# Performance work log

Measured on AMD Instinct MI355X. Metric: run time of the kernel, lower is better.

## Reference

```python
import jax, jax.numpy as jnp
import numpy as np
import math

N, M, D = 16384, 4096, 256
RATIO = 0.5
EDGE_PROB = 0.005  # ~80 nodes per hyperedge on average


def setup_inputs() -> dict:
    key = jax.random.key(0)
    k0, k1, k2, k3 = jax.random.split(key, 4)
    node_features = jax.random.normal(k0, (N, D), dtype=jnp.float32)
    # sparse-ish 0/1 incidence matrix, stored dense as in the original module
    incidence = (jax.random.uniform(k1, (N, M)) < EDGE_PROB).astype(jnp.float32)
    node_mask = jnp.ones((N,), dtype=bool)
    edge_mask = jnp.ones((M,), dtype=bool)
    W = (jax.random.normal(k2, (D, D)) / np.sqrt(D)).astype(jnp.float32)
    b = jnp.zeros((D,), dtype=jnp.float32)
    proj = (jax.random.normal(k3, (D,)) * 0.01).astype(jnp.float32)
    return dict(node_features=node_features, incidence=incidence,
                node_mask=node_mask, edge_mask=edge_mask,
                W=W, b=b, proj=proj)


def reference(node_features, incidence, node_mask, edge_mask, W, b, proj):
    n = node_features.shape[0]
    k = max(1, math.ceil(RATIO * n))  # static

    # --- UniGCNConv: node -> edge mean, edge -> node mean, then linear ---
    deg_e = jnp.clip(jnp.sum(incidence, axis=0), 1.0)          # [m]
    x_edge = (incidence.T @ node_features) / deg_e[:, None]     # [m, d]
    deg_v = jnp.clip(jnp.sum(incidence, axis=1), 1.0)           # [n]
    agg = (incidence @ x_edge) / deg_v[:, None]                 # [n, d]
    embeddings = agg @ W + b                                    # [n, d]

    # --- learned scalar score per node ---
    scores = jax.nn.sigmoid(embeddings @ proj)                  # [n]
    scores = jnp.where(node_mask, scores, -jnp.inf)

    # --- full argsort top-k -> boolean node mask (as in original) ---
    ranked = jnp.argsort(-scores)
    top_k_indices = ranked[:k]
    new_node_mask = jnp.zeros(n, dtype=jnp.bool_).at[top_k_indices].set(True)

    # --- gate features by score ---
    gated_features = node_features * scores[:, None]            # [n, d]

    # --- incidence masked-reduce -> active edges ---
    active_membership = incidence * new_node_mask[:, None].astype(incidence.dtype)
    edge_active_count = jnp.sum(active_membership, axis=0)      # [m]
    new_edge_mask = (edge_active_count > 0) & edge_mask

    return gated_features, new_node_mask, new_edge_mask
```

## Files before the change

kernel.cpp:

```cpp
#include <hip/hip_runtime.h>
#include <stdint.h>
#include <math.h>

#define N_NODES 16384
#define M_EDGES 4096
#define DFEAT   256
#define KSEL    8192
#define ECAP    192
#define VCAP    96


__global__ void build_lists(const float* __restrict__ inc,
                            int* __restrict__ ecnt, int* __restrict__ vcnt,
                            uint16_t* __restrict__ elist, uint16_t* __restrict__ vlist) {
    long long idx = (long long)blockIdx.x * blockDim.x + threadIdx.x;
    const long long total4 = (long long)N_NODES * M_EDGES / 4;
    if (idx >= total4) return;
    long long e = idx * 4;
    int n  = (int)(e >> 12);
    int m0 = (int)(e & 4095);
    const float4 v = ((const float4*)inc)[idx];
    float vals[4] = {v.x, v.y, v.z, v.w};
#pragma unroll
    for (int j = 0; j < 4; ++j) {
        if (vals[j] != 0.0f) {
            int m  = m0 + j;
            int ei = atomicAdd(&ecnt[m], 1);
            if (ei < ECAP) elist[(long long)m * ECAP + ei] = (uint16_t)n;
            int vi = atomicAdd(&vcnt[n], 1);
            if (vi < VCAP) vlist[(long long)n * VCAP + vi] = (uint16_t)m;
        }
    }
}

__global__ void compute_w2(const float* __restrict__ W, const float* __restrict__ b,
                           const float* __restrict__ proj, double* __restrict__ w2,
                           double* __restrict__ bp) {
    int d = threadIdx.x;
    double acc = 0.0;
    for (int j = 0; j < DFEAT; ++j)
        acc += (double)W[d * DFEAT + j] * (double)proj[j];
    w2[d] = acc;
    if (d == 0) {
        double s = 0.0;
        for (int j = 0; j < DFEAT; ++j) s += (double)b[j] * (double)proj[j];
        *bp = s;
    }
}

__global__ void z_kernel(const float* __restrict__ X, const double* __restrict__ w2,
                         double* __restrict__ z) {
    int wave = threadIdx.x >> 6;
    int lane = threadIdx.x & 63;
    int n = blockIdx.x * 4 + wave;
    float4 x = ((const float4*)X)[n * 64 + lane];
    int j = lane * 4;
    double acc = (double)x.x * w2[j] + (double)x.y * w2[j + 1]
               + (double)x.z * w2[j + 2] + (double)x.w * w2[j + 3];
    for (int o = 32; o > 0; o >>= 1) acc += __shfl_down(acc, o, 64);
    if (lane == 0) z[n] = acc;
}

__global__ void y_kernel(const double* __restrict__ z, const int* __restrict__ ecnt,
                         const uint16_t* __restrict__ elist, double* __restrict__ y) {
    int wave = threadIdx.x >> 6;
    int lane = threadIdx.x & 63;
    int m = blockIdx.x * 4 + wave;
    int cntr = ecnt[m];
    int cnt = cntr > ECAP ? ECAP : cntr;
    const uint16_t* lst = elist + (long long)m * ECAP;
    double acc = 0.0;
    for (int i = lane; i < cnt; i += 64) acc += z[lst[i]];
    for (int o = 32; o > 0; o >>= 1) acc += __shfl_down(acc, o, 64);
    if (lane == 0) {
        double deg = cntr > 0 ? (double)cntr : 1.0;
        y[m] = acc / deg;
    }
}

__global__ void logit_kernel(const double* __restrict__ y, const int* __restrict__ vcnt,
                             const uint16_t* __restrict__ vlist, const double* __restrict__ bp,
                             unsigned long long* __restrict__ keys, float* __restrict__ scores) {
    int n = blockIdx.x * blockDim.x + threadIdx.x;
    if (n >= N_NODES) return;
    int cntr = vcnt[n];
    int cnt = cntr > VCAP ? VCAP : cntr;
    const uint16_t* lst = vlist + (long long)n * VCAP;
    double acc = 0.0;
    for (int i = 0; i < cnt; ++i) acc += y[lst[i]];
    double deg = cntr > 0 ? (double)cntr : 1.0;
    double logit = acc / deg + *bp;
    scores[n] = (float)(1.0 / (1.0 + exp(-logit)));
    unsigned long long u = (unsigned long long)__double_as_longlong(logit);
    u = (u >> 63) ? ~u : (u | 0x8000000000000000ull);
    keys[n] = u;
}

__global__ __launch_bounds__(1024) void radix_select(
        const unsigned long long* __restrict__ keys, unsigned long long* __restrict__ Tu) {
    int tid = threadIdx.x;
    int wave = tid >> 6, lane = tid & 63;
    unsigned long long k[16];
#pragma unroll
    for (int i = 0; i < 16; ++i) k[i] = keys[i * 1024 + tid];
    __shared__ unsigned long long wsum[2][16];
    unsigned long long prefix = 0ull;
    int kr = KSEL;
    int par = 0;
    for (int shift = 62; shift >= 0; shift -= 2, par ^= 1) {
        unsigned long long base = prefix >> shift;
        int c3 = 0, c2 = 0, c1 = 0;
#pragma unroll
        for (int i = 0; i < 16; ++i) {
            unsigned long long hi = k[i] >> shift;
            c3 += (hi == base + 3);
            c2 += (hi == base + 2);
            c1 += (hi == base + 1);
        }
        unsigned long long packed = (unsigned long long)c3
                                  | ((unsigned long long)c2 << 21)
                                  | ((unsigned long long)c1 << 42);
        for (int o = 32; o > 0; o >>= 1) packed += __shfl_down(packed, o, 64);
        if (lane == 0) wsum[par][wave] = packed;
        __syncthreads();
        unsigned long long tot = 0;
#pragma unroll
        for (int w = 0; w < 16; ++w) tot += wsum[par][w];
        int n3 = (int)(tot & 0x1FFFFF);
        int n2 = (int)((tot >> 21) & 0x1FFFFF);
        int n1 = (int)((tot >> 42) & 0x1FFFFF);
        if (kr <= n3) prefix |= 3ull << shift;
        else { kr -= n3;
            if (kr <= n2) prefix |= 2ull << shift;
            else { kr -= n2;
                if (kr <= n1) prefix |= 1ull << shift;
                else kr -= n1;
            }
        }
    }
    if (tid == 0) *Tu = prefix;
}

__global__ __launch_bounds__(1024) void build_mask(
        const unsigned long long* __restrict__ keys, const unsigned long long* __restrict__ Tu,
        float* __restrict__ out_mask, int* __restrict__ maski) {
    int tid = threadIdx.x;
    int wave = tid >> 6, lane = tid & 63;
    unsigned long long T = *Tu;
    unsigned long long k[16];
#pragma unroll
    for (int i = 0; i < 16; ++i) k[i] = keys[tid * 16 + i];
    int ceq = 0, cgt = 0;
#pragma unroll
    for (int i = 0; i < 16; ++i) { cgt += (k[i] > T); ceq += (k[i] == T); }
    int eq_incl = ceq;
    for (int o = 1; o < 64; o <<= 1) {
        int v = __shfl_up(eq_incl, o, 64);
        if (lane >= o) eq_incl += v;
    }
    int gt_sum = cgt;
    for (int o = 32; o > 0; o >>= 1) gt_sum += __shfl_down(gt_sum, o, 64);
    __shared__ int weq[16], wgt[16];
    if (lane == 63) weq[wave] = eq_incl;
    if (lane == 0)  wgt[wave] = gt_sum;
    __syncthreads();
    int base_eq = 0, tot_gt = 0;
#pragma unroll
    for (int w = 0; w < 16; ++w) {
        if (w < wave) base_eq += weq[w];
        tot_gt += wgt[w];
    }
    int need = KSEL - tot_gt;
    int r = base_eq + eq_incl - ceq;
#pragma unroll
    for (int i = 0; i < 16; ++i) {
        bool eq = (k[i] == T);
        bool sel = (k[i] > T) || (eq && r < need);
        if (eq) ++r;
        int idx = tid * 16 + i;
        out_mask[idx] = sel ? 1.0f : 0.0f;
        maski[idx] = sel ? 1 : 0;
    }
}

__global__ void gated_out(const float* __restrict__ X, const float* __restrict__ scores,
                          float* __restrict__ out) {
    int idx = blockIdx.x * blockDim.x + threadIdx.x;
    int n = idx >> 6;
    float s = scores[n];
    float4 v = ((const float4*)X)[idx];
    v.x *= s; v.y *= s; v.z *= s; v.w *= s;
    ((float4*)out)[idx] = v;
}

__global__ void edge_mask_out(const int* __restrict__ ecnt, const uint16_t* __restrict__ elist,
                              const int* __restrict__ maski, float* __restrict__ out) {
    int m = blockIdx.x * blockDim.x + threadIdx.x;
    if (m >= M_EDGES) return;
    int cnt = ecnt[m]; if (cnt > ECAP) cnt = ECAP;
    const uint16_t* lst = elist + (long long)m * ECAP;
    int active = 0;
    for (int i = 0; i < cnt; ++i) {
        if (maski[lst[i]]) { active = 1; break; }
    }
    out[m] = active ? 1.0f : 0.0f;
}

extern "C" void kernel_launch(void* const* d_in, const int* in_sizes, int n_in,
                              void* d_out, int out_size, void* d_ws, size_t ws_size,
                              hipStream_t stream) {
    const float* X    = (const float*)d_in[0];
    const float* inc  = (const float*)d_in[1];
    const float* W    = (const float*)d_in[4];
    const float* b    = (const float*)d_in[5];
    const float* proj = (const float*)d_in[6];

    char* ws = (char*)d_ws;
    int*                ecnt   = (int*)(ws + 0);
    int*                vcnt   = (int*)(ws + 16384);
    double*             w2     = (double*)(ws + 81920);
    double*             bp     = (double*)(ws + 83968);
    unsigned long long* Tu     = (unsigned long long*)(ws + 83976);
    unsigned long long* keys   = (unsigned long long*)(ws + 131072);
    float*              scores = (float*)(ws + 262144);
    int*                maski  = (int*)(ws + 327680);
    double*             z      = (double*)(ws + 393216);
    double*             y      = (double*)(ws + 524288);
    uint16_t*           elist  = (uint16_t*)(ws + 4587520);
    uint16_t*           vlist  = (uint16_t*)(ws + 6160384);

    float* out_gated = (float*)d_out;
    float* out_nmask = out_gated + (long long)N_NODES * DFEAT;
    float* out_emask = out_nmask + N_NODES;

    hipMemsetAsync(ws, 0, 81920, stream);

    const long long total4 = (long long)N_NODES * M_EDGES / 4;
    build_lists<<<(int)(total4 / 256), 256, 0, stream>>>(inc, ecnt, vcnt, elist, vlist);
    compute_w2<<<1, 256, 0, stream>>>(W, b, proj, w2, bp);
    z_kernel<<<N_NODES / 4, 256, 0, stream>>>(X, w2, z);
    y_kernel<<<M_EDGES / 4, 256, 0, stream>>>(z, ecnt, elist, y);
    logit_kernel<<<N_NODES / 256, 256, 0, stream>>>(y, vcnt, vlist, bp, keys, scores);
    radix_select<<<1, 1024, 0, stream>>>(keys, Tu);
    build_mask<<<1, 1024, 0, stream>>>(keys, Tu, out_nmask, maski);
    gated_out<<<(N_NODES * DFEAT / 4) / 256, 256, 0, stream>>>(X, scores, out_gated);
    edge_mask_out<<<(M_EDGES + 255) / 256, 256, 0, stream>>>(ecnt, elist, maski, out_emask);
}
```

Measured before the change: 539.4 us.

## Fuse edge aggregation into row-wise incidence scan with atomic z accumulation

Replaces the per-element list builder plus per-edge gather with a single row-per-block kernel. It scans incidence, atomically accumulates node scalars into edge sums, and writes node adjacency lists using a wave prefix scan instead of per-node atomics. The edge list and separate y kernel are removed, and the edge mask is computed by scattering from selected nodes. The trade-off is contended fp64 atomics on edge sums and a summation order that is no longer deterministic.

```diff
diff --git a/kernel.cpp b/kernel.cpp
--- a/kernel.cpp
+++ b/kernel.cpp
@@ -6,32 +6,8 @@
 #define M_EDGES 4096
 #define DFEAT   256
 #define KSEL    8192
-#define ECAP    192
 #define VCAP    96
 
-
-__global__ void build_lists(const float* __restrict__ inc,
-                            int* __restrict__ ecnt, int* __restrict__ vcnt,
-                            uint16_t* __restrict__ elist, uint16_t* __restrict__ vlist) {
-    long long idx = (long long)blockIdx.x * blockDim.x + threadIdx.x;
-    const long long total4 = (long long)N_NODES * M_EDGES / 4;
-    if (idx >= total4) return;
-    long long e = idx * 4;
-    int n  = (int)(e >> 12);
-    int m0 = (int)(e & 4095);
-    const float4 v = ((const float4*)inc)[idx];
-    float vals[4] = {v.x, v.y, v.z, v.w};
-#pragma unroll
-    for (int j = 0; j < 4; ++j) {
-        if (vals[j] != 0.0f) {
-            int m  = m0 + j;
-            int ei = atomicAdd(&ecnt[m], 1);
-            if (ei < ECAP) elist[(long long)m * ECAP + ei] = (uint16_t)n;
-            int vi = atomicAdd(&vcnt[n], 1);
-            if (vi < VCAP) vlist[(long long)n * VCAP + vi] = (uint16_t)m;
-        }
-    }
-}
 
 __global__ void compute_w2(const float* __restrict__ W, const float* __restrict__ b,
                            const float* __restrict__ proj, double* __restrict__ w2,
@@ -61,24 +37,63 @@
     if (lane == 0) z[n] = acc;
 }
 
-__global__ void y_kernel(const double* __restrict__ z, const int* __restrict__ ecnt,
-                         const uint16_t* __restrict__ elist, double* __restrict__ y) {
-    int wave = threadIdx.x >> 6;
-    int lane = threadIdx.x & 63;
-    int m = blockIdx.x * 4 + wave;
-    int cntr = ecnt[m];
-    int cnt = cntr > ECAP ? ECAP : cntr;
-    const uint16_t* lst = elist + (long long)m * ECAP;
-    double acc = 0.0;
-    for (int i = lane; i < cnt; i += 64) acc += z[lst[i]];
-    for (int o = 32; o > 0; o >>= 1) acc += __shfl_down(acc, o, 64);
-    if (lane == 0) {
-        double deg = cntr > 0 ? (double)cntr : 1.0;
-        y[m] = acc / deg;
-    }
-}
-
-__global__ void logit_kernel(const double* __restrict__ y, const int* __restrict__ vcnt,
+__global__ void build(const float* __restrict__ inc, const double* __restrict__ z,
+                      int* __restrict__ ecnt, int* __restrict__ vcnt,
+                      double* __restrict__ ysum, uint16_t* __restrict__ vlist) {
+    int n = blockIdx.x;
+    int t = threadIdx.x;
+    int lane = t & 63, wv = t >> 6;
+    const float4* row4 = (const float4*)inc + (long long)n * 1024;
+    unsigned bits = 0;
+#pragma unroll
+    for (int c = 0; c < 4; ++c) {
+        float4 v = row4[c * 256 + t];
+        unsigned b = (v.x != 0.0f ? 1u : 0u) | (v.y != 0.0f ? 2u : 0u)
+                   | (v.z != 0.0f ? 4u : 0u) | (v.w != 0.0f ? 8u : 0u);
+        bits |= b << (c * 4);
+    }
+    double zn = z[n];
+    unsigned bb = bits;
+    while (bb) {
+        int k = __ffs(bb) - 1;
+        bb &= bb - 1;
+        int m = ((k >> 2) << 10) + t * 4 + (k & 3);
+        atomicAdd(&ysum[m], zn);
+        atomicAdd(&ecnt[m], 1);
+    }
+    int h = __popc(bits);
+    int incl = h;
+    for (int o = 1; o < 64; o <<= 1) {
+        int v = __shfl_up(incl, o, 64);
+        if (lane >= o) incl += v;
+    }
+    __shared__ int wtot[4];
+    if (lane == 63) wtot[wv] = incl;
+    __syncthreads();
+    int base = incl - h;
+#pragma unroll
+    for (int w = 0; w < 4; ++w) if (w < wv) base += wtot[w];
+    if (t == 0) vcnt[n] = wtot[0] + wtot[1] + wtot[2] + wtot[3];
+    uint16_t* vrow = vlist + (long long)n * VCAP;
+    int s = base;
+    while (bits) {
+        int k = __ffs(bits) - 1;
+        bits &= bits - 1;
+        int m = ((k >> 2) << 10) + t * 4 + (k & 3);
+        if (s < VCAP) vrow[s] = (uint16_t)m;
+        ++s;
+    }
+}
+
+__global__ void ymean_kernel(const double* __restrict__ ysum, const int* __restrict__ ecnt,
+                             double* __restrict__ ymean) {
+    int m = blockIdx.x * blockDim.x + threadIdx.x;
+    if (m >= M_EDGES) return;
+    int c = ecnt[m];
+    ymean[m] = ysum[m] / (c > 0 ? (double)c : 1.0);
+}
+
+__global__ void logit_kernel(const double* __restrict__ ymean, const int* __restrict__ vcnt,
                              const uint16_t* __restrict__ vlist, const double* __restrict__ bp,
                              unsigned long long* __restrict__ keys, float* __restrict__ scores) {
     int n = blockIdx.x * blockDim.x + threadIdx.x;
@@ -87,7 +102,7 @@
     int cnt = cntr > VCAP ? VCAP : cntr;
     const uint16_t* lst = vlist + (long long)n * VCAP;
     double acc = 0.0;
-    for (int i = 0; i < cnt; ++i) acc += y[lst[i]];
+    for (int i = 0; i < cnt; ++i) acc += ymean[lst[i]];
     double deg = cntr > 0 ? (double)cntr : 1.0;
     double logit = acc / deg + *bp;
     scores[n] = (float)(1.0 / (1.0 + exp(-logit)));
@@ -193,17 +208,14 @@
     ((float4*)out)[idx] = v;
 }
 
-__global__ void edge_mask_out(const int* __restrict__ ecnt, const uint16_t* __restrict__ elist,
-                              const int* __restrict__ maski, float* __restrict__ out) {
-    int m = blockIdx.x * blockDim.x + threadIdx.x;
-    if (m >= M_EDGES) return;
-    int cnt = ecnt[m]; if (cnt > ECAP) cnt = ECAP;
-    const uint16_t* lst = elist + (long long)m * ECAP;
-    int active = 0;
-    for (int i = 0; i < cnt; ++i) {
-        if (maski[lst[i]]) { active = 1; break; }
-    }
-    out[m] = active ? 1.0f : 0.0f;
+__global__ void emask_scatter(const int* __restrict__ maski, const int* __restrict__ vcnt,
+                              const uint16_t* __restrict__ vlist, float* __restrict__ out) {
+    int n = blockIdx.x * blockDim.x + threadIdx.x;
+    if (n >= N_NODES || !maski[n]) return;
+    int cntr = vcnt[n];
+    int cnt = cntr > VCAP ? VCAP : cntr;
+    const uint16_t* lst = vlist + (long long)n * VCAP;
+    for (int i = 0; i < cnt; ++i) out[lst[i]] = 1.0f;
 }
 
 extern "C" void kernel_launch(void* const* d_in, const int* in_sizes, int n_in,
@@ -218,31 +230,31 @@
     char* ws = (char*)d_ws;
     int*                ecnt   = (int*)(ws + 0);
     int*                vcnt   = (int*)(ws + 16384);
-    double*             w2     = (double*)(ws + 81920);
-    double*             bp     = (double*)(ws + 83968);
-    unsigned long long* Tu     = (unsigned long long*)(ws + 83976);
+    double*             ysum   = (double*)(ws + 81920);
+    double*             w2     = (double*)(ws + 114688);
+    double*             bp     = (double*)(ws + 116736);
+    unsigned long long* Tu     = (unsigned long long*)(ws + 116744);
     unsigned long long* keys   = (unsigned long long*)(ws + 131072);
     float*              scores = (float*)(ws + 262144);
     int*                maski  = (int*)(ws + 327680);
     double*             z      = (double*)(ws + 393216);
-    double*             y      = (double*)(ws + 524288);
-    uint16_t*           elist  = (uint16_t*)(ws + 4587520);
-    uint16_t*           vlist  = (uint16_t*)(ws + 6160384);
+    double*             ymean  = (double*)(ws + 524288);
+    uint16_t*           vlist  = (uint16_t*)(ws + 557056);
 
     float* out_gated = (float*)d_out;
     float* out_nmask = out_gated + (long long)N_NODES * DFEAT;
     float* out_emask = out_nmask + N_NODES;
 
-    hipMemsetAsync(ws, 0, 81920, stream);
-
-    const long long total4 = (long long)N_NODES * M_EDGES / 4;
-    build_lists<<<(int)(total4 / 256), 256, 0, stream>>>(inc, ecnt, vcnt, elist, vlist);
+    hipMemsetAsync(ws, 0, 114688, stream);
+    hipMemsetAsync(out_emask, 0, M_EDGES * sizeof(float), stream);
+
     compute_w2<<<1, 256, 0, stream>>>(W, b, proj, w2, bp);
     z_kernel<<<N_NODES / 4, 256, 0, stream>>>(X, w2, z);
-    y_kernel<<<M_EDGES / 4, 256, 0, stream>>>(z, ecnt, elist, y);
-    logit_kernel<<<N_NODES / 256, 256, 0, stream>>>(y, vcnt, vlist, bp, keys, scores);
+    build<<<N_NODES, 256, 0, stream>>>(inc, z, ecnt, vcnt, ysum, vlist);
+    ymean_kernel<<<M_EDGES / 256, 256, 0, stream>>>(ysum, ecnt, ymean);
+    logit_kernel<<<N_NODES / 256, 256, 0, stream>>>(ymean, vcnt, vlist, bp, keys, scores);
     radix_select<<<1, 1024, 0, stream>>>(keys, Tu);
     build_mask<<<1, 1024, 0, stream>>>(keys, Tu, out_nmask, maski);
     gated_out<<<(N_NODES * DFEAT / 4) / 256, 256, 0, stream>>>(X, scores, out_gated);
-    edge_mask_out<<<(M_EDGES + 255) / 256, 256, 0, stream>>>(ecnt, elist, maski, out_emask);
-}
+    emask_scatter<<<N_NODES / 256, 256, 0, stream>>>(maski, vcnt, vlist, out_emask);
+}
```

New measurement: 490.6 us. 9.0% less time.
